# Optimization experiments

Hardware: AMD Instinct MI355X
Metric: run time of the kernel (lower is better)

The kernel has to match this reference:

```python
import jax, jax.numpy as jnp
import numpy as np

N, E, B, D, H, L = 50000, 800000, 16, 64, 128, 2


def _lin(h, w, b):
    return h @ w + b


def _scatter_mean(v, idx, n):
    s = jax.ops.segment_sum(v, idx, num_segments=n)
    c = jax.ops.segment_sum(jnp.ones((v.shape[0],), v.dtype), idx, num_segments=n)
    return s / jnp.maximum(c, 1.0)[:, None]


def setup_inputs() -> dict:
    key = jax.random.key(0)
    ks = iter(jax.random.split(key, 40))

    def p(*shape):
        return jax.random.normal(next(ks), shape, dtype=jnp.float32) * 0.05

    inp = {
        "x": jax.random.normal(next(ks), (N, D), dtype=jnp.float32),
        "edge_attr": jax.random.normal(next(ks), (E, D), dtype=jnp.float32),
        "u": jax.random.normal(next(ks), (B, D), dtype=jnp.float32),
        "e_w1": p(L, 4 * D, H), "e_b1": p(L, H),
        "e_w2": p(L, H, H), "e_b2": p(L, H),
        "e_w3": p(L, H, D), "e_b3": p(L, D),
        "n1_w1": p(L, 2 * D, H), "n1_b1": p(L, H),
        "n1_w2": p(L, H, H), "n1_b2": p(L, H),
        "n2_w1": p(L, D + H + D, H), "n2_b1": p(L, H),
        "n2_w2": p(L, H, D), "n2_b2": p(L, D),
        "g_w1": p(L, 3 * D, H), "g_b1": p(L, H),
        "g_w2": p(L, H, D), "g_b2": p(L, D),
        "edge_index": jax.random.randint(next(ks), (2, E), 0, N, dtype=jnp.int32),
        "batch": jnp.sort(jax.random.randint(next(ks), (N,), 0, B, dtype=jnp.int32)),
    }
    return inp


def _forward(x, edge_attr, u, params, edge_index, batch):
    row, col = edge_index[0], edge_index[1]
    eb = batch[row]  # [E] graph id per edge
    x0, e0, u0 = x, edge_attr, u
    for l in range(L):
        (e_w1, e_b1, e_w2, e_b2, e_w3, e_b3,
         n1_w1, n1_b1, n1_w2, n1_b2,
         n2_w1, n2_b1, n2_w2, n2_b2,
         g_w1, g_b1, g_w2, g_b2) = [pm[l] for pm in params]
        # Edge model: [E, e+2n+u] -> MLP -> [E, D]
        h = jnp.concatenate([x[row], x[col], edge_attr, u[eb]], axis=1)
        h = jax.nn.relu(_lin(h, e_w1, e_b1))
        h = jax.nn.relu(_lin(h, e_w2, e_b2))
        edge_attr = _lin(h, e_w3, e_b3)
        # Node model: gather src node + edge, MLP1, scatter_mean onto dest, MLP2
        se = jnp.concatenate([x[row], edge_attr], axis=1)  # [E, 2D]
        se = _lin(jax.nn.relu(_lin(se, n1_w1, n1_b1)), n1_w2, n1_b2)
        agg = _scatter_mean(se, col, N)  # [N, H]
        xh = jnp.concatenate([x, agg, u[batch]], axis=1)
        x = _lin(jax.nn.relu(_lin(xh, n2_w1, n2_b1)), n2_w2, n2_b2)
        # Global model: per-graph means of updated nodes/edges
        e_agg = _scatter_mean(edge_attr, eb, B)
        n_agg = _scatter_mean(x, batch, B)
        uh = jnp.concatenate([u, n_agg, e_agg], axis=1)
        u = _lin(jax.nn.relu(_lin(uh, g_w1, g_b1)), g_w2, g_b2)
    return x + x0, edge_attr + e0, u + u0


def reference(x, edge_attr, u, e_w1, e_b1, e_w2, e_b2, e_w3, e_b3, n1_w1, n1_b1, n1_w2, n1_b2, n2_w1, n2_b1, n2_w2, n2_b2, g_w1, g_b1, g_w2, g_b2, edge_index, batch):
    params = (e_w1, e_b1, e_w2, e_b2, e_w3, e_b3,
              n1_w1, n1_b1, n1_w2, n1_b2,
              n2_w1, n2_b1, n2_w2, n2_b2,
              g_w1, g_b1, g_w2, g_b2)
    return _forward(x, edge_attr, u, params, edge_index, batch)
```

## Files before the change

### kernel.cpp

```cpp
#include <hip/hip_runtime.h>

#define N_NODES 50000
#define E_EDGES 800000
#define NG 16
#define DD 64
#define HH 128

typedef __attribute__((ext_vector_type(8))) __bf16 bf16x8;
typedef __attribute__((ext_vector_type(4))) float f32x4;
typedef unsigned int uint;
typedef __attribute__((ext_vector_type(4))) uint uint4v;

#define MFMA16(a,b,c) __builtin_amdgcn_mfma_f32_16x16x32_bf16((a),(b),(c),0,0,0)

__device__ __forceinline__ unsigned short f2bf(float f){
  uint u = __builtin_bit_cast(uint, f);
  u += 0x7fffu + ((u >> 16) & 1u);
  return (unsigned short)(u >> 16);
}
__device__ __forceinline__ uint pk2(float a, float b){
  return (uint)f2bf(a) | ((uint)f2bf(b) << 16);
}

__device__ __forceinline__ bf16x8 ldfrag(const char* base, int row, int byteoff){
  uint4v v = *(const uint4v*)(base + row*256 + (byteoff ^ ((row & 7) << 4)));
  return __builtin_bit_cast(bf16x8, v);
}
__device__ __forceinline__ void st_h(char* base, int row, int col, float v){
  *(unsigned short*)(base + row*256 + ((col*2) ^ ((row & 7) << 4))) = f2bf(v);
}
__device__ __forceinline__ void st_chunk(char* base, int row, int c16, uint4v v){
  *(uint4v*)(base + row*256 + ((c16*16) ^ ((row & 7) << 4))) = v;
}

__device__ __forceinline__ void stage_b(char* sB, const unsigned short* wt,
                                        int Nout, int Ktot, int koff, int t){
  for (int task = t; task < Nout*16; task += 256){
    int n = task >> 4, c = task & 15;
    uint4v v = *(const uint4v*)(wt + (long)n*Ktot + koff + c*8);
    st_chunk(sB, n, c, v);
  }
}

template<int NT>
__device__ __forceinline__ void gemm_acc(const char* Abase, const char* Bbase,
                                         int wv, int l15, int lhi, f32x4* acc){
  #pragma unroll
  for (int kt = 0; kt < 4; ++kt){
    bf16x8 a = ldfrag(Abase, wv*16 + l15, kt*64 + lhi*16);
    #pragma unroll
    for (int n = 0; n < NT; ++n){
      bf16x8 bb = ldfrag(Bbase, n*16 + l15, kt*64 + lhi*16);
      acc[n] = MFMA16(a, bb, acc[n]);
    }
  }
}

template<int NT, bool RELU>
__device__ __forceinline__ void epi_lds(char* dst, const f32x4* acc, const float* bias,
                                        int wv, int l15, int lhi){
  #pragma unroll
  for (int n = 0; n < NT; ++n){
    float bv = bias[n*16 + l15];
    #pragma unroll
    for (int j = 0; j < 4; ++j){
      int r = wv*16 + lhi*4 + j;
      float v = acc[n][j] + bv;
      if (RELU) v = fmaxf(v, 0.f);
      st_h(dst, r, n*16 + l15, v);
    }
  }
}

__global__ void pack_weights(const float* __restrict__ e1, const float* __restrict__ e2,
                             const float* __restrict__ e3, const float* __restrict__ n11,
                             const float* __restrict__ n12, const float* __restrict__ n21,
                             const float* __restrict__ n22, unsigned short* __restrict__ out){
  int idx = blockIdx.x * 256 + threadIdx.x;
  int l = idx / 131072, r = idx % 131072;
  const float* src; int K, N, off;
  if      (r <  32768){ src = e1;  K = 256; N = 128; off = 0; }
  else if (r <  49152){ src = e2;  K = 128; N = 128; off = 32768; }
  else if (r <  57344){ src = e3;  K = 128; N = 64;  off = 49152; }
  else if (r <  73728){ src = n11; K = 128; N = 128; off = 57344; }
  else if (r <  90112){ src = n12; K = 128; N = 128; off = 73728; }
  else if (r < 122880){ src = n21; K = 256; N = 128; off = 90112; }
  else                { src = n22; K = 128; N = 64;  off = 122880; }
  int q = r - off; int k = q / N; int n = q % N;
  out[(long)l*131072 + off + n*K + k] = f2bf(src[(long)l*K*N + q]);
}

__global__ void count_kernel(const int* __restrict__ edge_index, const int* __restrict__ batch,
                             float* __restrict__ cnt_col, float* __restrict__ cnt_eb){
  __shared__ float h[NG];
  int t = threadIdx.x;
  if (t < NG) h[t] = 0.f;
  __syncthreads();
  int e = blockIdx.x * 256 + t;
  if (e < E_EDGES){
    atomicAdd(cnt_col + edge_index[E_EDGES + e], 1.f);
    atomicAdd(&h[batch[edge_index[e]]], 1.f);
  }
  __syncthreads();
  if (t < NG) atomicAdd(cnt_eb + t, h[t]);
}
__global__ void count_nodes_kernel(const int* __restrict__ batch, float* __restrict__ cnt_b){
  __shared__ float h[NG];
  int t = threadIdx.x;
  if (t < NG) h[t] = 0.f;
  __syncthreads();
  int n = blockIdx.x * 256 + t;
  if (n < N_NODES) atomicAdd(&h[batch[n]], 1.f);
  __syncthreads();
  if (t < NG) atomicAdd(cnt_b + t, h[t]);
}

__global__ __launch_bounds__(256, 2) void edge_kernel(
    const float* __restrict__ x_cur, const float* __restrict__ e_cur,
    const float* __restrict__ u_cur, const float* __restrict__ e_resid,
    const int* __restrict__ edge_index, const int* __restrict__ batch,
    const unsigned short* __restrict__ w_e1, const unsigned short* __restrict__ w_e2,
    const unsigned short* __restrict__ w_e3, const unsigned short* __restrict__ w_n11,
    const unsigned short* __restrict__ w_n12,
    const float* __restrict__ b_e1, const float* __restrict__ b_e2,
    const float* __restrict__ b_e3, const float* __restrict__ b_n11,
    const float* __restrict__ b_n12,
    float* __restrict__ e_out, float* __restrict__ agg_sum, float* __restrict__ e_agg,
    int has_resid)
{
  __shared__ __align__(16) char sA[16384];
  __shared__ __align__(16) char sB[32768];
  __shared__ __align__(16) char sH[16384];
  __shared__ int sRow[64], sCol[64], sEb[64];
  __shared__ float sEagg[NG*DD];

  const int t = threadIdx.x;
  const int wv = t >> 6, ln = t & 63, l15 = ln & 15, lhi = ln >> 4;
  const int ebase = blockIdx.x * 64;

  if (t < 64){
    int r = edge_index[ebase + t];
    int c = edge_index[E_EDGES + ebase + t];
    sRow[t] = r; sCol[t] = c; sEb[t] = batch[r];
  }
  for (int i = t; i < NG*DD; i += 256) sEagg[i] = 0.f;
  __syncthreads();

  f32x4 acc1[8];
  #pragma unroll
  for (int n = 0; n < 8; ++n) acc1[n] = f32x4{0.f,0.f,0.f,0.f};

  for (int half = 0; half < 2; ++half){
    for (int task = t; task < 1024; task += 256){
      int r = task >> 4, c = task & 15;
      const float* src;
      if (half == 0) src = (c < 8) ? (x_cur + (long)sRow[r]*DD + c*8)
                                   : (x_cur + (long)sCol[r]*DD + (c-8)*8);
      else           src = (c < 8) ? (e_cur + (long)(ebase + r)*DD + c*8)
                                   : (u_cur + (long)sEb[r]*DD + (c-8)*8);
      float4 lo = *(const float4*)src;
      float4 hi = *(const float4*)(src + 4);
      uint4v v; v.x = pk2(lo.x, lo.y); v.y = pk2(lo.z, lo.w);
      v.z = pk2(hi.x, hi.y); v.w = pk2(hi.z, hi.w);
      st_chunk(sA, r, c, v);
    }
    stage_b(sB, w_e1, 128, 256, half*128, t);
    __syncthreads();
    gemm_acc<8>(sA, sB, wv, l15, lhi, acc1);
    __syncthreads();
  }
  epi_lds<8, true>(sH, acc1, b_e1, wv, l15, lhi);
  stage_b(sB, w_e2, 128, 128, 0, t);
  __syncthreads();

  f32x4 acc2[8];
  #pragma unroll
  for (int n = 0; n < 8; ++n) acc2[n] = f32x4{0.f,0.f,0.f,0.f};
  gemm_acc<8>(sH, sB, wv, l15, lhi, acc2);
  __syncthreads();
  epi_lds<8, true>(sA, acc2, b_e2, wv, l15, lhi);
  stage_b(sB, w_e3, 64, 128, 0, t);
  __syncthreads();

  f32x4 acc3[4];
  #pragma unroll
  for (int n = 0; n < 4; ++n) acc3[n] = f32x4{0.f,0.f,0.f,0.f};
  gemm_acc<4>(sA, sB, wv, l15, lhi, acc3);

  float enew[4][4];
  #pragma unroll
  for (int n = 0; n < 4; ++n){
    float bv = b_e3[n*16 + l15];
    #pragma unroll
    for (int j = 0; j < 4; ++j){
      int r = wv*16 + lhi*4 + j;
      int col = n*16 + l15;
      float v = acc3[n][j] + bv;
      enew[n][j] = v;
      long eg = (long)(ebase + r)*DD + col;
      e_out[eg] = has_resid ? (v + e_resid[eg]) : v;
      atomicAdd(&sEagg[sEb[r]*DD + col], v);
    }
  }
  __syncthreads();

  #pragma unroll
  for (int n = 0; n < 4; ++n){
    #pragma unroll
    for (int j = 0; j < 4; ++j){
      int r = wv*16 + lhi*4 + j;
      st_h(sA, r, 64 + n*16 + l15, enew[n][j]);
    }
  }
  for (int task = t; task < 512; task += 256){
    int r = task >> 3, c = task & 7;
    const float* src = x_cur + (long)sRow[r]*DD + c*8;
    float4 lo = *(const float4*)src;
    float4 hi = *(const float4*)(src + 4);
    uint4v v; v.x = pk2(lo.x, lo.y); v.y = pk2(lo.z, lo.w);
    v.z = pk2(hi.x, hi.y); v.w = pk2(hi.z, hi.w);
    st_chunk(sA, r, c, v);
  }
  stage_b(sB, w_n11, 128, 128, 0, t);
  __syncthreads();

  f32x4 acc4[8];
  #pragma unroll
  for (int n = 0; n < 8; ++n) acc4[n] = f32x4{0.f,0.f,0.f,0.f};
  gemm_acc<8>(sA, sB, wv, l15, lhi, acc4);
  __syncthreads();
  epi_lds<8, true>(sH, acc4, b_n11, wv, l15, lhi);
  stage_b(sB, w_n12, 128, 128, 0, t);
  __syncthreads();

  f32x4 acc5[8];
  #pragma unroll
  for (int n = 0; n < 8; ++n) acc5[n] = f32x4{0.f,0.f,0.f,0.f};
  gemm_acc<8>(sH, sB, wv, l15, lhi, acc5);

  #pragma unroll
  for (int n = 0; n < 8; ++n){
    float bv = b_n12[n*16 + l15];
    #pragma unroll
    for (int j = 0; j < 4; ++j){
      int r = wv*16 + lhi*4 + j;
      float v = acc5[n][j] + bv;
      atomicAdd(agg_sum + (long)sCol[r]*HH + n*16 + l15, v);
    }
  }
  for (int i = t; i < NG*DD; i += 256) atomicAdd(e_agg + i, sEagg[i]);
}

__global__ __launch_bounds__(256, 2) void node_kernel(
    const float* __restrict__ x_cur, const float* __restrict__ u_cur,
    const float* __restrict__ x_resid, const int* __restrict__ batch,
    const float* __restrict__ agg_sum, const float* __restrict__ cnt_col,
    const unsigned short* __restrict__ w_n21, const unsigned short* __restrict__ w_n22,
    const float* __restrict__ b_n21, const float* __restrict__ b_n22,
    float* __restrict__ x_out, float* __restrict__ n_agg, int has_resid)
{
  __shared__ __align__(16) char sA[16384];
  __shared__ __align__(16) char sB[32768];
  __shared__ __align__(16) char sH[16384];
  __shared__ int sBat[64];
  __shared__ float sRinv[64];
  __shared__ float sNagg[NG*DD];

  const int t = threadIdx.x;
  const int wv = t >> 6, ln = t & 63, l15 = ln & 15, lhi = ln >> 4;
  const int n0 = blockIdx.x * 64;

  if (t < 64){
    int nd = n0 + t;
    int ok = nd < N_NODES;
    sBat[t] = ok ? batch[nd] : 0;
    float c = ok ? cnt_col[nd] : 1.f;
    sRinv[t] = 1.f / fmaxf(c, 1.f);
  }
  for (int i = t; i < NG*DD; i += 256) sNagg[i] = 0.f;
  __syncthreads();

  f32x4 acc[8];
  #pragma unroll
  for (int n = 0; n < 8; ++n) acc[n] = f32x4{0.f,0.f,0.f,0.f};

  for (int half = 0; half < 2; ++half){
    for (int task = t; task < 1024; task += 256){
      int r = task >> 4, c = task & 15;
      int nd = n0 + r;
      bool ok = nd < N_NODES;
      float scale = 1.f;
      const float* src;
      if (half == 0){
        if (c < 8) src = x_cur + (long)nd*DD + c*8;
        else { src = agg_sum + (long)nd*HH + (c-8)*8; scale = sRinv[r]; }
      } else {
        if (c < 8){ src = agg_sum + (long)nd*HH + 64 + c*8; scale = sRinv[r]; }
        else src = u_cur + (long)sBat[r]*DD + (c-8)*8;
      }
      float4 lo = {0.f,0.f,0.f,0.f}, hi = {0.f,0.f,0.f,0.f};
      if (ok){ lo = *(const float4*)src; hi = *(const float4*)(src + 4); }
      uint4v v; v.x = pk2(lo.x*scale, lo.y*scale); v.y = pk2(lo.z*scale, lo.w*scale);
      v.z = pk2(hi.x*scale, hi.y*scale); v.w = pk2(hi.z*scale, hi.w*scale);
      st_chunk(sA, r, c, v);
    }
    stage_b(sB, w_n21, 128, 256, half*128, t);
    __syncthreads();
    gemm_acc<8>(sA, sB, wv, l15, lhi, acc);
    __syncthreads();
  }
  epi_lds<8, true>(sH, acc, b_n21, wv, l15, lhi);
  stage_b(sB, w_n22, 64, 128, 0, t);
  __syncthreads();

  f32x4 acc2[4];
  #pragma unroll
  for (int n = 0; n < 4; ++n) acc2[n] = f32x4{0.f,0.f,0.f,0.f};
  gemm_acc<4>(sH, sB, wv, l15, lhi, acc2);

  #pragma unroll
  for (int n = 0; n < 4; ++n){
    float bv = b_n22[n*16 + l15];
    #pragma unroll
    for (int j = 0; j < 4; ++j){
      int r = wv*16 + lhi*4 + j;
      int nd = n0 + r;
      if (nd < N_NODES){
        int col = n*16 + l15;
        float v = acc2[n][j] + bv;
        long xg = (long)nd*DD + col;
        x_out[xg] = has_resid ? (v + x_resid[xg]) : v;
        atomicAdd(&sNagg[sBat[r]*DD + col], v);
      }
    }
  }
  __syncthreads();
  for (int i = t; i < NG*DD; i += 256) atomicAdd(n_agg + i, sNagg[i]);
}

__global__ void global_kernel(const float* __restrict__ u_cur, const float* __restrict__ n_agg,
                              const float* __restrict__ e_agg, const float* __restrict__ cnt_b,
                              const float* __restrict__ cnt_e,
                              const float* __restrict__ g_w1, const float* __restrict__ g_b1,
                              const float* __restrict__ g_w2, const float* __restrict__ g_b2,
                              const float* __restrict__ u_resid, float* __restrict__ u_out,
                              int has_resid)
{
  int g = blockIdx.x, t = threadIdx.x;
  __shared__ float uh[192];
  __shared__ float hb[128];
  float v;
  if (t < 64)       v = u_cur[g*64 + t];
  else if (t < 128) v = n_agg[g*64 + (t-64)] / fmaxf(cnt_b[g], 1.f);
  else              v = e_agg[g*64 + (t-128)] / fmaxf(cnt_e[g], 1.f);
  uh[t] = v;
  __syncthreads();
  if (t < 128){
    float s = g_b1[t];
    for (int k = 0; k < 192; ++k) s += uh[k] * g_w1[k*128 + t];
    hb[t] = fmaxf(s, 0.f);
  }
  __syncthreads();
  if (t < 64){
    float s = g_b2[t];
    for (int k = 0; k < 128; ++k) s += hb[k] * g_w2[k*64 + t];
    if (has_resid) s += u_resid[g*64 + t];
    u_out[g*64 + t] = s;
  }
}

extern "C" void kernel_launch(void* const* d_in, const int* in_sizes, int n_in,
                              void* d_out, int out_size, void* d_ws, size_t ws_size,
                              hipStream_t stream)
{
  const float* x0   = (const float*)d_in[0];
  const float* e0   = (const float*)d_in[1];
  const float* u0   = (const float*)d_in[2];
  const float* e_w1 = (const float*)d_in[3];
  const float* e_b1 = (const float*)d_in[4];
  const float* e_w2 = (const float*)d_in[5];
  const float* e_b2 = (const float*)d_in[6];
  const float* e_w3 = (const float*)d_in[7];
  const float* e_b3 = (const float*)d_in[8];
  const float* n1_w1 = (const float*)d_in[9];
  const float* n1_b1 = (const float*)d_in[10];
  const float* n1_w2 = (const float*)d_in[11];
  const float* n1_b2 = (const float*)d_in[12];
  const float* n2_w1 = (const float*)d_in[13];
  const float* n2_b1 = (const float*)d_in[14];
  const float* n2_w2 = (const float*)d_in[15];
  const float* n2_b2 = (const float*)d_in[16];
  const float* g_w1 = (const float*)d_in[17];
  const float* g_b1 = (const float*)d_in[18];
  const float* g_w2 = (const float*)d_in[19];
  const float* g_b2 = (const float*)d_in[20];
  const int* edge_index = (const int*)d_in[21];
  const int* batch      = (const int*)d_in[22];

  float* out_x = (float*)d_out;
  float* out_e = out_x + (long)N_NODES*DD;
  float* out_u = out_e + (long)E_EDGES*DD;

  char* ws = (char*)d_ws;
  float* agg_sum = (float*)ws;
  float* cnt_col = (float*)(ws + 25600000);
  float* cnt_eb  = (float*)(ws + 25800000);
  float* cnt_b   = (float*)(ws + 25800064);
  float* e_agg   = (float*)(ws + 25800128);
  float* n_agg   = (float*)(ws + 25804224);
  unsigned short* packed = (unsigned short*)(ws + 25808320);

  (void)hipMemsetAsync(cnt_col, 0, 200128, stream);
  pack_weights<<<1024, 256, 0, stream>>>(e_w1, e_w2, e_w3, n1_w1, n1_w2, n2_w1, n2_w2, packed);
  count_kernel<<<3125, 256, 0, stream>>>(edge_index, batch, cnt_col, cnt_eb);
  count_nodes_kernel<<<196, 256, 0, stream>>>(batch, cnt_b);

  const float* xc = x0;
  const float* ec = e0;
  const float* uc = u0;
  for (int l = 0; l < 2; ++l){
    (void)hipMemsetAsync(agg_sum, 0, (size_t)N_NODES*HH*4, stream);
    (void)hipMemsetAsync(e_agg, 0, 4096, stream);
    (void)hipMemsetAsync(n_agg, 0, 4096, stream);
    const unsigned short* P = packed + (long)l*131072;
    edge_kernel<<<E_EDGES/64, 256, 0, stream>>>(
        xc, ec, uc, e0, edge_index, batch,
        P + 0, P + 32768, P + 49152, P + 57344, P + 73728,
        e_b1 + l*128, e_b2 + l*128, e_b3 + l*64, n1_b1 + l*128, n1_b2 + l*128,
        out_e, agg_sum, e_agg, l == 1);
    node_kernel<<<782, 256, 0, stream>>>(
        xc, uc, x0, batch, agg_sum, cnt_col,
        P + 90112, P + 122880, n2_b1 + l*128, n2_b2 + l*64,
        out_x, n_agg, l == 1);
    global_kernel<<<NG, 192, 0, stream>>>(
        uc, n_agg, e_agg, cnt_b, cnt_eb,
        g_w1 + l*192*128, g_b1 + l*128, g_w2 + l*128*64, g_b2 + l*64,
        u0, out_u, l == 1);
    xc = out_x; ec = out_e; uc = out_u;
  }
}
```

Baseline: 2.067 ms.

## Replace scatter-add atomics with CSR-ordered bf16 buffer and node-side gather

Builds a CSR ordering of edges by destination node once (degree histogram, multi-block scan, atomic fill of each edge's slot). The edge kernel then writes each edge's node-MLP1 output as bf16 rows into that slot instead of issuing 128 float atomics per edge into agg_sum. The node kernel sums its incoming rows in registers and divides by the degree itself. Separately, the edge kernel moves to 512 threads, with the 8 waves splitting the output columns in halves. The cost is a roughly 205 MB workspace buffer with extra write/read traffic and bf16 rounding of the messages before summation, and the path is only taken when the workspace is large enough.

```diff
diff --git a/kernel.cpp b/kernel.cpp
--- a/kernel.cpp
+++ b/kernel.cpp
@@ -5,57 +5,99 @@
 #define NG 16
 #define DD 64
 #define HH 128
+#define NB_SCAN 49
 
 typedef __attribute__((ext_vector_type(8))) __bf16 bf16x8;
 typedef __attribute__((ext_vector_type(4))) float f32x4;
 typedef unsigned int uint;
+typedef unsigned short ushort;
 typedef __attribute__((ext_vector_type(4))) uint uint4v;
 
 #define MFMA16(a,b,c) __builtin_amdgcn_mfma_f32_16x16x32_bf16((a),(b),(c),0,0,0)
 
-__device__ __forceinline__ unsigned short f2bf(float f){
+__device__ __forceinline__ ushort f2bf(float f){
   uint u = __builtin_bit_cast(uint, f);
   u += 0x7fffu + ((u >> 16) & 1u);
-  return (unsigned short)(u >> 16);
+  return (ushort)(u >> 16);
 }
 __device__ __forceinline__ uint pk2(float a, float b){
   return (uint)f2bf(a) | ((uint)f2bf(b) << 16);
 }
+__device__ __forceinline__ float bflo(uint u){ return __builtin_bit_cast(float, u << 16); }
+__device__ __forceinline__ float bfhi(uint u){ return __builtin_bit_cast(float, u & 0xffff0000u); }
 
 __device__ __forceinline__ bf16x8 ldfrag(const char* base, int row, int byteoff){
   uint4v v = *(const uint4v*)(base + row*256 + (byteoff ^ ((row & 7) << 4)));
   return __builtin_bit_cast(bf16x8, v);
 }
+__device__ __forceinline__ uint4v ld_chunk(const char* base, int row, int c16){
+  return *(const uint4v*)(base + row*256 + ((c16*16) ^ ((row & 7) << 4)));
+}
 __device__ __forceinline__ void st_h(char* base, int row, int col, float v){
-  *(unsigned short*)(base + row*256 + ((col*2) ^ ((row & 7) << 4))) = f2bf(v);
+  *(ushort*)(base + row*256 + ((col*2) ^ ((row & 7) << 4))) = f2bf(v);
 }
 __device__ __forceinline__ void st_chunk(char* base, int row, int c16, uint4v v){
   *(uint4v*)(base + row*256 + ((c16*16) ^ ((row & 7) << 4))) = v;
 }
-
-__device__ __forceinline__ void stage_b(char* sB, const unsigned short* wt,
-                                        int Nout, int Ktot, int koff, int t){
-  for (int task = t; task < Nout*16; task += 256){
+__device__ __forceinline__ void pack16(char* dst, int r, int c16, const float* src){
+  float4 lo = *(const float4*)src;
+  float4 hi = *(const float4*)(src + 4);
+  uint4v v; v.x = pk2(lo.x, lo.y); v.y = pk2(lo.z, lo.w);
+  v.z = pk2(hi.x, hi.y); v.w = pk2(hi.z, hi.w);
+  st_chunk(dst, r, c16, v);
+}
+
+__device__ __forceinline__ void stage_b(char* sB, const ushort* wt,
+                                        int Nout, int Ktot, int koff, int t, int stride){
+  for (int task = t; task < Nout*16; task += stride){
     int n = task >> 4, c = task & 15;
     uint4v v = *(const uint4v*)(wt + (long)n*Ktot + koff + c*8);
     st_chunk(sB, n, c, v);
   }
 }
 
+__device__ __forceinline__ void gemmN4(const char* A, const char* B,
+                                       int mw, int nh, int l15, int lhi, f32x4* acc){
+  #pragma unroll
+  for (int kt = 0; kt < 4; ++kt){
+    bf16x8 a = ldfrag(A, mw*16 + l15, kt*64 + lhi*16);
+    #pragma unroll
+    for (int n = 0; n < 4; ++n){
+      bf16x8 bb = ldfrag(B, (nh*4 + n)*16 + l15, kt*64 + lhi*16);
+      acc[n] = MFMA16(a, bb, acc[n]);
+    }
+  }
+}
+template<bool RELU>
+__device__ __forceinline__ void epiN4(char* dst, const f32x4* acc, const float* bias,
+                                      int mw, int nh, int l15, int lhi){
+  #pragma unroll
+  for (int n = 0; n < 4; ++n){
+    int col = nh*64 + n*16 + l15;
+    float bv = bias[col];
+    #pragma unroll
+    for (int j = 0; j < 4; ++j){
+      int r = mw*16 + lhi*4 + j;
+      float v = acc[n][j] + bv;
+      if (RELU) v = fmaxf(v, 0.f);
+      st_h(dst, r, col, v);
+    }
+  }
+}
+
 template<int NT>
-__device__ __forceinline__ void gemm_acc(const char* Abase, const char* Bbase,
+__device__ __forceinline__ void gemm_acc(const char* A, const char* B,
                                          int wv, int l15, int lhi, f32x4* acc){
   #pragma unroll
   for (int kt = 0; kt < 4; ++kt){
-    bf16x8 a = ldfrag(Abase, wv*16 + l15, kt*64 + lhi*16);
+    bf16x8 a = ldfrag(A, wv*16 + l15, kt*64 + lhi*16);
     #pragma unroll
     for (int n = 0; n < NT; ++n){
-      bf16x8 bb = ldfrag(Bbase, n*16 + l15, kt*64 + lhi*16);
+      bf16x8 bb = ldfrag(B, n*16 + l15, kt*64 + lhi*16);
       acc[n] = MFMA16(a, bb, acc[n]);
     }
   }
 }
-
 template<int NT, bool RELU>
 __device__ __forceinline__ void epi_lds(char* dst, const f32x4* acc, const float* bias,
                                         int wv, int l15, int lhi){
@@ -75,7 +117,7 @@
 __global__ void pack_weights(const float* __restrict__ e1, const float* __restrict__ e2,
                              const float* __restrict__ e3, const float* __restrict__ n11,
                              const float* __restrict__ n12, const float* __restrict__ n21,
-                             const float* __restrict__ n22, unsigned short* __restrict__ out){
+                             const float* __restrict__ n22, ushort* __restrict__ out){
   int idx = blockIdx.x * 256 + threadIdx.x;
   int l = idx / 131072, r = idx % 131072;
   const float* src; int K, N, off;
@@ -90,15 +132,15 @@
   out[(long)l*131072 + off + n*K + k] = f2bf(src[(long)l*K*N + q]);
 }
 
-__global__ void count_kernel(const int* __restrict__ edge_index, const int* __restrict__ batch,
-                             float* __restrict__ cnt_col, float* __restrict__ cnt_eb){
+__global__ void hist_kernel(const int* __restrict__ edge_index, const int* __restrict__ batch,
+                            int* __restrict__ deg, float* __restrict__ cnt_eb){
   __shared__ float h[NG];
   int t = threadIdx.x;
   if (t < NG) h[t] = 0.f;
   __syncthreads();
   int e = blockIdx.x * 256 + t;
   if (e < E_EDGES){
-    atomicAdd(cnt_col + edge_index[E_EDGES + e], 1.f);
+    atomicAdd(deg + edge_index[E_EDGES + e], 1);
     atomicAdd(&h[batch[edge_index[e]]], 1.f);
   }
   __syncthreads();
@@ -114,19 +156,64 @@
   __syncthreads();
   if (t < NG) atomicAdd(cnt_b + t, h[t]);
 }
-
-__global__ __launch_bounds__(256, 2) void edge_kernel(
+__global__ void scan_a(const int* __restrict__ deg, int* __restrict__ bsum){
+  __shared__ int red[1024];
+  int i = blockIdx.x*1024 + threadIdx.x;
+  red[threadIdx.x] = (i < N_NODES) ? deg[i] : 0;
+  __syncthreads();
+  for (int s = 512; s > 0; s >>= 1){
+    if ((int)threadIdx.x < s) red[threadIdx.x] += red[threadIdx.x + s];
+    __syncthreads();
+  }
+  if (threadIdx.x == 0) bsum[blockIdx.x] = red[0];
+}
+__global__ void scan_b(const int* __restrict__ bsum, int* __restrict__ bbase){
+  if (threadIdx.x == 0){
+    int run = 0;
+    for (int b = 0; b < NB_SCAN; ++b){ int v = bsum[b]; bbase[b] = run; run += v; }
+  }
+}
+__global__ void scan_c(const int* __restrict__ deg, const int* __restrict__ bbase,
+                       int* __restrict__ off, int* __restrict__ cursor){
+  __shared__ int sc[1024];
+  int i = blockIdx.x*1024 + threadIdx.x;
+  int v = (i < N_NODES) ? deg[i] : 0;
+  sc[threadIdx.x] = v;
+  __syncthreads();
+  for (int d = 1; d < 1024; d <<= 1){
+    int add = ((int)threadIdx.x >= d) ? sc[threadIdx.x - d] : 0;
+    __syncthreads();
+    sc[threadIdx.x] += add;
+    __syncthreads();
+  }
+  if (i < N_NODES){
+    int ex = sc[threadIdx.x] - v + bbase[blockIdx.x];
+    off[i] = ex; cursor[i] = ex;
+  }
+}
+__global__ void fill_kernel(const int* __restrict__ edge_index, int* __restrict__ cursor,
+                            int* __restrict__ pos){
+  int e = blockIdx.x*256 + threadIdx.x;
+  if (e < E_EDGES){
+    int c = edge_index[E_EDGES + e];
+    pos[e] = atomicAdd(&cursor[c], 1);
+  }
+}
+
+template<bool CSR>
+__global__ __launch_bounds__(512, 4) void edge_kernel(
     const float* __restrict__ x_cur, const float* __restrict__ e_cur,
     const float* __restrict__ u_cur, const float* __restrict__ e_resid,
     const int* __restrict__ edge_index, const int* __restrict__ batch,
-    const unsigned short* __restrict__ w_e1, const unsigned short* __restrict__ w_e2,
-    const unsigned short* __restrict__ w_e3, const unsigned short* __restrict__ w_n11,
-    const unsigned short* __restrict__ w_n12,
+    const int* __restrict__ pos_arr,
+    const ushort* __restrict__ w_e1, const ushort* __restrict__ w_e2,
+    const ushort* __restrict__ w_e3, const ushort* __restrict__ w_n11,
+    const ushort* __restrict__ w_n12,
     const float* __restrict__ b_e1, const float* __restrict__ b_e2,
     const float* __restrict__ b_e3, const float* __restrict__ b_n11,
     const float* __restrict__ b_n12,
-    float* __restrict__ e_out, float* __restrict__ agg_sum, float* __restrict__ e_agg,
-    int has_resid)
+    float* __restrict__ e_out, ushort* __restrict__ se_buf,
+    float* __restrict__ agg_sum, float* __restrict__ e_agg, int has_resid)
 {
   __shared__ __align__(16) char sA[16384];
   __shared__ __align__(16) char sB[32768];
@@ -136,65 +223,66 @@
 
   const int t = threadIdx.x;
   const int wv = t >> 6, ln = t & 63, l15 = ln & 15, lhi = ln >> 4;
+  const int mw = wv & 3, nh = wv >> 2;
   const int ebase = blockIdx.x * 64;
 
   if (t < 64){
     int r = edge_index[ebase + t];
-    int c = edge_index[E_EDGES + ebase + t];
-    sRow[t] = r; sCol[t] = c; sEb[t] = batch[r];
-  }
-  for (int i = t; i < NG*DD; i += 256) sEagg[i] = 0.f;
-  __syncthreads();
-
-  f32x4 acc1[8];
-  #pragma unroll
-  for (int n = 0; n < 8; ++n) acc1[n] = f32x4{0.f,0.f,0.f,0.f};
-
-  for (int half = 0; half < 2; ++half){
-    for (int task = t; task < 1024; task += 256){
+    sRow[t] = r; sCol[t] = edge_index[E_EDGES + ebase + t]; sEb[t] = batch[r];
+  }
+  for (int i = t; i < NG*DD; i += 512) sEagg[i] = 0.f;
+  __syncthreads();
+
+  f32x4 acc1[4];
+  #pragma unroll
+  for (int n = 0; n < 4; ++n) acc1[n] = f32x4{0.f,0.f,0.f,0.f};
+  for (int kh = 0; kh < 2; ++kh){
+    for (int task = t; task < 1024; task += 512){
       int r = task >> 4, c = task & 15;
       const float* src;
-      if (half == 0) src = (c < 8) ? (x_cur + (long)sRow[r]*DD + c*8)
-                                   : (x_cur + (long)sCol[r]*DD + (c-8)*8);
-      else           src = (c < 8) ? (e_cur + (long)(ebase + r)*DD + c*8)
-                                   : (u_cur + (long)sEb[r]*DD + (c-8)*8);
-      float4 lo = *(const float4*)src;
-      float4 hi = *(const float4*)(src + 4);
-      uint4v v; v.x = pk2(lo.x, lo.y); v.y = pk2(lo.z, lo.w);
-      v.z = pk2(hi.x, hi.y); v.w = pk2(hi.z, hi.w);
-      st_chunk(sA, r, c, v);
-    }
-    stage_b(sB, w_e1, 128, 256, half*128, t);
-    __syncthreads();
-    gemm_acc<8>(sA, sB, wv, l15, lhi, acc1);
-    __syncthreads();
-  }
-  epi_lds<8, true>(sH, acc1, b_e1, wv, l15, lhi);
-  stage_b(sB, w_e2, 128, 128, 0, t);
-  __syncthreads();
-
-  f32x4 acc2[8];
-  #pragma unroll
-  for (int n = 0; n < 8; ++n) acc2[n] = f32x4{0.f,0.f,0.f,0.f};
-  gemm_acc<8>(sH, sB, wv, l15, lhi, acc2);
-  __syncthreads();
-  epi_lds<8, true>(sA, acc2, b_e2, wv, l15, lhi);
-  stage_b(sB, w_e3, 64, 128, 0, t);
-  __syncthreads();
-
-  f32x4 acc3[4];
-  #pragma unroll
-  for (int n = 0; n < 4; ++n) acc3[n] = f32x4{0.f,0.f,0.f,0.f};
-  gemm_acc<4>(sA, sB, wv, l15, lhi, acc3);
-
-  float enew[4][4];
-  #pragma unroll
-  for (int n = 0; n < 4; ++n){
-    float bv = b_e3[n*16 + l15];
+      if (kh == 0) src = (c < 8) ? (x_cur + (long)sRow[r]*DD + c*8)
+                                 : (x_cur + (long)sCol[r]*DD + (c-8)*8);
+      else         src = (c < 8) ? (e_cur + (long)(ebase + r)*DD + c*8)
+                                 : (u_cur + (long)sEb[r]*DD + (c-8)*8);
+      pack16(sA, r, c, src);
+    }
+    stage_b(sB, w_e1, 128, 256, kh*128, t, 512);
+    __syncthreads();
+    gemmN4(sA, sB, mw, nh, l15, lhi, acc1);
+    __syncthreads();
+  }
+  epiN4<true>(sH, acc1, b_e1, mw, nh, l15, lhi);
+  stage_b(sB, w_e2, 128, 128, 0, t, 512);
+  __syncthreads();
+
+  f32x4 acc2[4];
+  #pragma unroll
+  for (int n = 0; n < 4; ++n) acc2[n] = f32x4{0.f,0.f,0.f,0.f};
+  gemmN4(sH, sB, mw, nh, l15, lhi, acc2);
+  __syncthreads();
+  epiN4<true>(sA, acc2, b_e2, mw, nh, l15, lhi);
+  stage_b(sB, w_e3, 64, 128, 0, t, 512);
+  __syncthreads();
+
+  f32x4 acc3[2];
+  acc3[0] = f32x4{0.f,0.f,0.f,0.f}; acc3[1] = f32x4{0.f,0.f,0.f,0.f};
+  #pragma unroll
+  for (int kt = 0; kt < 4; ++kt){
+    bf16x8 a = ldfrag(sA, mw*16 + l15, kt*64 + lhi*16);
+    #pragma unroll
+    for (int n = 0; n < 2; ++n){
+      bf16x8 bb = ldfrag(sB, (nh*2 + n)*16 + l15, kt*64 + lhi*16);
+      acc3[n] = MFMA16(a, bb, acc3[n]);
+    }
+  }
+  float enew[2][4];
+  #pragma unroll
+  for (int n = 0; n < 2; ++n){
+    int col = nh*32 + n*16 + l15;
+    float bv = b_e3[col];
     #pragma unroll
     for (int j = 0; j < 4; ++j){
-      int r = wv*16 + lhi*4 + j;
-      int col = n*16 + l15;
+      int r = mw*16 + lhi*4 + j;
       float v = acc3[n][j] + bv;
       enew[n][j] = v;
       long eg = (long)(ebase + r)*DD + col;
@@ -205,64 +293,70 @@
   __syncthreads();
 
   #pragma unroll
-  for (int n = 0; n < 4; ++n){
+  for (int n = 0; n < 2; ++n){
     #pragma unroll
     for (int j = 0; j < 4; ++j){
-      int r = wv*16 + lhi*4 + j;
-      st_h(sA, r, 64 + n*16 + l15, enew[n][j]);
-    }
-  }
-  for (int task = t; task < 512; task += 256){
-    int r = task >> 3, c = task & 7;
-    const float* src = x_cur + (long)sRow[r]*DD + c*8;
-    float4 lo = *(const float4*)src;
-    float4 hi = *(const float4*)(src + 4);
-    uint4v v; v.x = pk2(lo.x, lo.y); v.y = pk2(lo.z, lo.w);
-    v.z = pk2(hi.x, hi.y); v.w = pk2(hi.z, hi.w);
-    st_chunk(sA, r, c, v);
-  }
-  stage_b(sB, w_n11, 128, 128, 0, t);
-  __syncthreads();
-
-  f32x4 acc4[8];
-  #pragma unroll
-  for (int n = 0; n < 8; ++n) acc4[n] = f32x4{0.f,0.f,0.f,0.f};
-  gemm_acc<8>(sA, sB, wv, l15, lhi, acc4);
-  __syncthreads();
-  epi_lds<8, true>(sH, acc4, b_n11, wv, l15, lhi);
-  stage_b(sB, w_n12, 128, 128, 0, t);
-  __syncthreads();
-
-  f32x4 acc5[8];
-  #pragma unroll
-  for (int n = 0; n < 8; ++n) acc5[n] = f32x4{0.f,0.f,0.f,0.f};
-  gemm_acc<8>(sH, sB, wv, l15, lhi, acc5);
-
-  #pragma unroll
-  for (int n = 0; n < 8; ++n){
-    float bv = b_n12[n*16 + l15];
-    #pragma unroll
-    for (int j = 0; j < 4; ++j){
-      int r = wv*16 + lhi*4 + j;
-      float v = acc5[n][j] + bv;
-      atomicAdd(agg_sum + (long)sCol[r]*HH + n*16 + l15, v);
-    }
-  }
-  for (int i = t; i < NG*DD; i += 256) atomicAdd(e_agg + i, sEagg[i]);
-}
-
+      int r = mw*16 + lhi*4 + j;
+      st_h(sA, r, 64 + nh*32 + n*16 + l15, enew[n][j]);
+    }
+  }
+  { int r = t >> 3, c = t & 7;
+    pack16(sA, r, c, x_cur + (long)sRow[r]*DD + c*8); }
+  stage_b(sB, w_n11, 128, 128, 0, t, 512);
+  __syncthreads();
+
+  f32x4 acc4[4];
+  #pragma unroll
+  for (int n = 0; n < 4; ++n) acc4[n] = f32x4{0.f,0.f,0.f,0.f};
+  gemmN4(sA, sB, mw, nh, l15, lhi, acc4);
+  __syncthreads();
+  epiN4<true>(sH, acc4, b_n11, mw, nh, l15, lhi);
+  stage_b(sB, w_n12, 128, 128, 0, t, 512);
+  __syncthreads();
+
+  f32x4 acc5[4];
+  #pragma unroll
+  for (int n = 0; n < 4; ++n) acc5[n] = f32x4{0.f,0.f,0.f,0.f};
+  gemmN4(sH, sB, mw, nh, l15, lhi, acc5);
+
+  if (CSR){
+    epiN4<false>(sA, acc5, b_n12, mw, nh, l15, lhi);
+    __syncthreads();
+    int r = t >> 3, oct = t & 7;
+    long p = pos_arr[ebase + r];
+    uint4v v0 = ld_chunk(sA, r, oct*2);
+    uint4v v1 = ld_chunk(sA, r, oct*2 + 1);
+    *(uint4v*)(se_buf + p*128 + oct*16) = v0;
+    *(uint4v*)(se_buf + p*128 + oct*16 + 8) = v1;
+  } else {
+    #pragma unroll
+    for (int n = 0; n < 4; ++n){
+      int col = nh*64 + n*16 + l15;
+      float bv = b_n12[col];
+      #pragma unroll
+      for (int j = 0; j < 4; ++j){
+        int r = mw*16 + lhi*4 + j;
+        atomicAdd(agg_sum + (long)sCol[r]*HH + col, acc5[n][j] + bv);
+      }
+    }
+  }
+  for (int i = t; i < NG*DD; i += 512) atomicAdd(e_agg + i, sEagg[i]);
+}
+
+template<bool CSR>
 __global__ __launch_bounds__(256, 2) void node_kernel(
     const float* __restrict__ x_cur, const float* __restrict__ u_cur,
     const float* __restrict__ x_resid, const int* __restrict__ batch,
-    const float* __restrict__ agg_sum, const float* __restrict__ cnt_col,
-    const unsigned short* __restrict__ w_n21, const unsigned short* __restrict__ w_n22,
+    const ushort* __restrict__ se_buf, const int* __restrict__ deg,
+    const int* __restrict__ off, const float* __restrict__ agg_sum,
+    const ushort* __restrict__ w_n21, const ushort* __restrict__ w_n22,
     const float* __restrict__ b_n21, const float* __restrict__ b_n22,
     float* __restrict__ x_out, float* __restrict__ n_agg, int has_resid)
 {
   __shared__ __align__(16) char sA[16384];
   __shared__ __align__(16) char sB[32768];
   __shared__ __align__(16) char sH[16384];
-  __shared__ int sBat[64];
+  __shared__ int sBat[64], sDeg[64], sOff[64];
   __shared__ float sRinv[64];
   __shared__ float sNagg[NG*DD];
 
@@ -274,43 +368,95 @@
     int nd = n0 + t;
     int ok = nd < N_NODES;
     sBat[t] = ok ? batch[nd] : 0;
-    float c = ok ? cnt_col[nd] : 1.f;
-    sRinv[t] = 1.f / fmaxf(c, 1.f);
+    int d = ok ? deg[nd] : 0;
+    sDeg[t] = d;
+    sOff[t] = ok ? off[nd] : 0;
+    sRinv[t] = 1.f / fmaxf((float)d, 1.f);
   }
   for (int i = t; i < NG*DD; i += 256) sNagg[i] = 0.f;
   __syncthreads();
 
+  float s[32];
+  const int r4 = t >> 2, q = t & 3;
+  if (CSR){
+    #pragma unroll
+    for (int k = 0; k < 32; ++k) s[k] = 0.f;
+    int d = sDeg[r4], o = sOff[r4];
+    for (int i = 0; i < d; ++i){
+      const ushort* src = se_buf + (long)(o + i)*HH + q*32;
+      #pragma unroll
+      for (int c = 0; c < 4; ++c){
+        uint4v v = *(const uint4v*)(src + c*8);
+        #pragma unroll
+        for (int jj = 0; jj < 4; ++jj){
+          s[c*8 + jj*2]     += bflo(v[jj]);
+          s[c*8 + jj*2 + 1] += bfhi(v[jj]);
+        }
+      }
+    }
+    float riv = sRinv[r4];
+    #pragma unroll
+    for (int k = 0; k < 32; ++k) s[k] *= riv;
+  }
+
   f32x4 acc[8];
   #pragma unroll
   for (int n = 0; n < 8; ++n) acc[n] = f32x4{0.f,0.f,0.f,0.f};
 
   for (int half = 0; half < 2; ++half){
-    for (int task = t; task < 1024; task += 256){
-      int r = task >> 4, c = task & 15;
-      int nd = n0 + r;
-      bool ok = nd < N_NODES;
-      float scale = 1.f;
-      const float* src;
-      if (half == 0){
-        if (c < 8) src = x_cur + (long)nd*DD + c*8;
-        else { src = agg_sum + (long)nd*HH + (c-8)*8; scale = sRinv[r]; }
-      } else {
-        if (c < 8){ src = agg_sum + (long)nd*HH + 64 + c*8; scale = sRinv[r]; }
-        else src = u_cur + (long)sBat[r]*DD + (c-8)*8;
+    if (CSR){
+      for (int task = t; task < 512; task += 256){
+        int r = task >> 3, c = task & 7;
+        int nd = n0 + r;
+        bool ok = nd < N_NODES;
+        float4 lo = {0,0,0,0}, hi = {0,0,0,0};
+        if (ok){
+          const float* src = (half == 0) ? (x_cur + (long)nd*DD + c*8)
+                                         : (u_cur + (long)sBat[r]*DD + c*8);
+          lo = *(const float4*)src; hi = *(const float4*)(src + 4);
+        }
+        uint4v v; v.x = pk2(lo.x, lo.y); v.y = pk2(lo.z, lo.w);
+        v.z = pk2(hi.x, hi.y); v.w = pk2(hi.z, hi.w);
+        st_chunk(sA, r, (half == 0) ? c : (8 + c), v);
       }
-      float4 lo = {0.f,0.f,0.f,0.f}, hi = {0.f,0.f,0.f,0.f};
-      if (ok){ lo = *(const float4*)src; hi = *(const float4*)(src + 4); }
-      uint4v v; v.x = pk2(lo.x*scale, lo.y*scale); v.y = pk2(lo.z*scale, lo.w*scale);
-      v.z = pk2(hi.x*scale, hi.y*scale); v.w = pk2(hi.z*scale, hi.w*scale);
-      st_chunk(sA, r, c, v);
-    }
-    stage_b(sB, w_n21, 128, 256, half*128, t);
+      if ((half == 0 && q < 2) || (half == 1 && q >= 2)){
+        int cbase = (half == 0) ? (8 + q*4) : ((q - 2)*4);
+        #pragma unroll
+        for (int cc = 0; cc < 4; ++cc){
+          uint4v v;
+          v.x = pk2(s[cc*8+0], s[cc*8+1]); v.y = pk2(s[cc*8+2], s[cc*8+3]);
+          v.z = pk2(s[cc*8+4], s[cc*8+5]); v.w = pk2(s[cc*8+6], s[cc*8+7]);
+          st_chunk(sA, r4, cbase + cc, v);
+        }
+      }
+    } else {
+      for (int task = t; task < 1024; task += 256){
+        int r = task >> 4, c = task & 15;
+        int nd = n0 + r;
+        bool ok = nd < N_NODES;
+        float scale = 1.f;
+        const float* src;
+        if (half == 0){
+          if (c < 8) src = x_cur + (long)nd*DD + c*8;
+          else { src = agg_sum + (long)nd*HH + (c-8)*8; scale = sRinv[r]; }
+        } else {
+          if (c < 8){ src = agg_sum + (long)nd*HH + 64 + c*8; scale = sRinv[r]; }
+          else src = u_cur + (long)sBat[r]*DD + (c-8)*8;
+        }
+        float4 lo = {0,0,0,0}, hi = {0,0,0,0};
+        if (ok){ lo = *(const float4*)src; hi = *(const float4*)(src + 4); }
+        uint4v v; v.x = pk2(lo.x*scale, lo.y*scale); v.y = pk2(lo.z*scale, lo.w*scale);
+        v.z = pk2(hi.x*scale, hi.y*scale); v.w = pk2(hi.z*scale, hi.w*scale);
+        st_chunk(sA, r, c, v);
+      }
+    }
+    stage_b(sB, w_n21, 128, 256, half*128, t, 256);
     __syncthreads();
     gemm_acc<8>(sA, sB, wv, l15, lhi, acc);
     __syncthreads();
   }
   epi_lds<8, true>(sH, acc, b_n21, wv, l15, lhi);
-  stage_b(sB, w_n22, 64, 128, 0, t);
+  stage_b(sB, w_n22, 64, 128, 0, t, 256);
   __syncthreads();
 
   f32x4 acc2[4];
@@ -402,36 +548,63 @@
   float* out_u = out_e + (long)E_EDGES*DD;
 
   char* ws = (char*)d_ws;
-  float* agg_sum = (float*)ws;
-  float* cnt_col = (float*)(ws + 25600000);
-  float* cnt_eb  = (float*)(ws + 25800000);
-  float* cnt_b   = (float*)(ws + 25800064);
-  float* e_agg   = (float*)(ws + 25800128);
-  float* n_agg   = (float*)(ws + 25804224);
-  unsigned short* packed = (unsigned short*)(ws + 25808320);
-
-  (void)hipMemsetAsync(cnt_col, 0, 200128, stream);
+  int*   deg    = (int*)(ws + 0);
+  int*   off    = (int*)(ws + 200000);
+  int*   cursor = (int*)(ws + 400000);
+  int*   bsum   = (int*)(ws + 600000);
+  int*   bbase  = (int*)(ws + 600256);
+  float* cnt_eb = (float*)(ws + 600512);
+  float* cnt_b  = (float*)(ws + 600576);
+  float* e_agg  = (float*)(ws + 600640);
+  float* n_agg  = (float*)(ws + 604736);
+  ushort* packed = (ushort*)(ws + 608832);
+  const size_t big = 1133120;
+  bool use_csr = ws_size >= (size_t)(big + 204800000 + 3200000);
+  ushort* se_buf = (ushort*)(ws + big);
+  int*    pos    = (int*)(ws + big + 204800000);
+  float*  agg_sum = (float*)(ws + big);
+
+  (void)hipMemsetAsync(deg, 0, 200000, stream);
+  (void)hipMemsetAsync(cnt_eb, 0, 128, stream);
   pack_weights<<<1024, 256, 0, stream>>>(e_w1, e_w2, e_w3, n1_w1, n1_w2, n2_w1, n2_w2, packed);
-  count_kernel<<<3125, 256, 0, stream>>>(edge_index, batch, cnt_col, cnt_eb);
+  hist_kernel<<<3125, 256, 0, stream>>>(edge_index, batch, deg, cnt_eb);
   count_nodes_kernel<<<196, 256, 0, stream>>>(batch, cnt_b);
+  if (use_csr){
+    scan_a<<<NB_SCAN, 1024, 0, stream>>>(deg, bsum);
+    scan_b<<<1, 64, 0, stream>>>(bsum, bbase);
+    scan_c<<<NB_SCAN, 1024, 0, stream>>>(deg, bbase, off, cursor);
+    fill_kernel<<<3125, 256, 0, stream>>>(edge_index, cursor, pos);
+  }
 
   const float* xc = x0;
   const float* ec = e0;
   const float* uc = u0;
   for (int l = 0; l < 2; ++l){
-    (void)hipMemsetAsync(agg_sum, 0, (size_t)N_NODES*HH*4, stream);
-    (void)hipMemsetAsync(e_agg, 0, 4096, stream);
-    (void)hipMemsetAsync(n_agg, 0, 4096, stream);
-    const unsigned short* P = packed + (long)l*131072;
-    edge_kernel<<<E_EDGES/64, 256, 0, stream>>>(
-        xc, ec, uc, e0, edge_index, batch,
-        P + 0, P + 32768, P + 49152, P + 57344, P + 73728,
-        e_b1 + l*128, e_b2 + l*128, e_b3 + l*64, n1_b1 + l*128, n1_b2 + l*128,
-        out_e, agg_sum, e_agg, l == 1);
-    node_kernel<<<782, 256, 0, stream>>>(
-        xc, uc, x0, batch, agg_sum, cnt_col,
-        P + 90112, P + 122880, n2_b1 + l*128, n2_b2 + l*64,
-        out_x, n_agg, l == 1);
+    (void)hipMemsetAsync(e_agg, 0, 8192, stream);
+    if (!use_csr)
+      (void)hipMemsetAsync(agg_sum, 0, (size_t)N_NODES*HH*4, stream);
+    const ushort* P = packed + (long)l*131072;
+    if (use_csr){
+      edge_kernel<true><<<E_EDGES/64, 512, 0, stream>>>(
+          xc, ec, uc, e0, edge_index, batch, pos,
+          P + 0, P + 32768, P + 49152, P + 57344, P + 73728,
+          e_b1 + l*128, e_b2 + l*128, e_b3 + l*64, n1_b1 + l*128, n1_b2 + l*128,
+          out_e, se_buf, agg_sum, e_agg, l == 1);
+      node_kernel<true><<<782, 256, 0, stream>>>(
+          xc, uc, x0, batch, se_buf, deg, off, agg_sum,
+          P + 90112, P + 122880, n2_b1 + l*128, n2_b2 + l*64,
+          out_x, n_agg, l == 1);
+    } else {
+      edge_kernel<false><<<E_EDGES/64, 512, 0, stream>>>(
+          xc, ec, uc, e0, edge_index, batch, pos,
+          P + 0, P + 32768, P + 49152, P + 57344, P + 73728,
+          e_b1 + l*128, e_b2 + l*128, e_b3 + l*64, n1_b1 + l*128, n1_b2 + l*128,
+          out_e, se_buf, agg_sum, e_agg, l == 1);
+      node_kernel<false><<<782, 256, 0, stream>>>(
+          xc, uc, x0, batch, se_buf, deg, off, agg_sum,
+          P + 90112, P + 122880, n2_b1 + l*128, n2_b2 + l*64,
+          out_x, n_agg, l == 1);
+    }
     global_kernel<<<NG, 192, 0, stream>>>(
         uc, n_agg, e_agg, cnt_b, cnt_eb,
         g_w1 + l*192*128, g_b1 + l*128, g_w2 + l*128*64, g_b2 + l*64,
```

After: 1.805 ms. -12.7%, faster.
